# Kernel tuning notes

Measured on AMD Instinct MI355X. Metric: run time of the kernel, lower is better.

## Reference

```python
import jax, jax.numpy as jnp
import numpy as np

EPS = 1e-6

def _det3(m):
    return (m[..., 0, 0] * m[..., 1, 1] * m[..., 2, 2]
            + m[..., 0, 1] * m[..., 1, 2] * m[..., 2, 0]
            + m[..., 1, 0] * m[..., 2, 1] * m[..., 0, 2]
            - m[..., 2, 0] * m[..., 1, 1] * m[..., 0, 2]
            - m[..., 0, 0] * m[..., 2, 1] * m[..., 1, 2]
            - m[..., 1, 0] * m[..., 0, 1] * m[..., 2, 2])

def _inv3(m):
    a, b, c = m[..., 0, 0], m[..., 0, 1], m[..., 0, 2]
    d, e, f = m[..., 1, 0], m[..., 1, 1], m[..., 1, 2]
    g, h, i = m[..., 2, 0], m[..., 2, 1], m[..., 2, 2]
    adj = jnp.stack([
        jnp.stack([e * i - f * h, c * h - b * i, b * f - c * e], -1),
        jnp.stack([f * g - d * i, a * i - c * g, c * d - a * f], -1),
        jnp.stack([d * h - e * g, b * g - a * h, a * e - b * d], -1)], -2)
    return adj / _det3(m)[..., None, None]

def setup_inputs() -> dict:
    key = jax.random.key(0)
    ks = jax.random.split(key, 12)
    N, B, DH = 100000, 2048, 256
    idx = jnp.sort(jnp.concatenate([jnp.arange(B, dtype=jnp.int32),
                                    jax.random.randint(ks[0], (N - B,), 0, B, dtype=jnp.int32)]))
    return {
        "t": jax.random.uniform(ks[1], (B, 1), jnp.float32, 0.01, 0.99),
        "h": jax.random.normal(ks[2], (N, DH), jnp.float32),
        "pos": jax.random.normal(ks[3], (N, 3), jnp.float32),
        "eps_h": jax.random.normal(ks[4], (N, DH), jnp.float32),
        "eps_pos": jax.random.normal(ks[5], (N, 3), jnp.float32),
        "gparam_h": jax.random.normal(ks[6], (1, 1), jnp.float32),
        "gparam_pos": jax.random.normal(ks[7], (1, 1), jnp.float32),
        "W_mu": jax.random.normal(ks[8], (DH, DH), jnp.float32) / np.sqrt(DH),
        "W_r1": jax.random.normal(ks[9], (DH, 2 * DH), jnp.float32) / np.sqrt(DH),
        "W_r2": jax.random.normal(ks[10], (2 * DH, DH), jnp.float32) / np.sqrt(2 * DH),
        "index": idx,
        "num_graphs": B,
    }


def _forward(t, h, pos, eps_h, eps_pos, gparam_h, gparam_pos, W_mu, W_r1, W_r2, index, B):
    eye = jnp.eye(3, dtype=h.dtype)
    seg_sum = lambda x: jax.ops.segment_sum(x, index, num_segments=B)
    counts = seg_sum(jnp.ones((index.shape[0],), h.dtype))  # [B]

    def scatter_center(x):  # x - per-graph mean, gathered back
        mean = seg_sum(x) / counts[:, None]
        return x - mean[index]

    # volatility g(t): per-graph, gathered to nodes
    g_h = (0.1 + jax.nn.softplus(gparam_h) * t)[index]      # [N,1]
    g_pos = (0.1 + jax.nn.softplus(gparam_pos) * t)[index]  # [N,1]

    def f_net(t_, hh, pp):  # surrogate forward transformation f
        tn = t_[index]                                      # [N,1]
        mu_h = (hh @ W_mu) * (1.0 - tn)
        sigma_h = 0.1 + 0.9 * tn                            # [N,1]
        mu_pos = pp * (1.0 - tn)
        nrm = pp / (jnp.linalg.norm(pp, axis=-1, keepdims=True) + EPS)
        a = (0.2 + 0.8 * tn)[..., None]                     # [N,1,1]
        b = (0.1 * tn)[..., None]
        U = a * eye + b * (nrm[:, :, None] * nrm[:, None, :])  # [N,3,3]
        return mu_h, sigma_h, mu_pos, U

    def z_pos_fn(mu, U, eps):
        return mu + scatter_center(jnp.einsum('nij,nj->ni', U, eps))

    def score_pos_fn(eps, U, inv_U=None, C=None):
        if inv_U is None or C is None:
            inv_U = _inv3(U)
            inv_V = _inv3(seg_sum(inv_U))
            C = inv_V[index] @ (inv_U - eye)
        y = jnp.einsum('nji,nj->ni', inv_U, eps)
        ybar = seg_sum(y)
        c = jnp.einsum('nji,nj->ni', C, ybar[index])
        return scatter_center(c - y)  # zero_cog_score=True

    def solve_pos_fn(U, prel):
        inv_U = _inv3(U)
        inv_V = _inv3(seg_sum(inv_U))
        C = inv_V[index] @ (inv_U - eye)
        c = seg_sum(jnp.einsum('nij,nj->ni', C, prel))[index]
        eps = jnp.einsum('nij,nj->ni', inv_U, prel - c)
        return eps, inv_U, C

    bdrift = lambda dz, score, g: dz - 0.5 * g ** 2 * score

    # ---- target backward drift (time_derivative via jvp over t) ----
    (mu_h, sig_h, mu_p, U), (dmu_h, dsig_h, dmu_p, dU) = jax.jvp(
        lambda tt: f_net(tt, h, pos), (t,), (jnp.ones_like(t),))
    z_h = mu_h + sig_h * eps_h
    dz_h = dmu_h + dsig_h * eps_h
    z_p = z_pos_fn(mu_p, U, eps_pos)
    dz_p = z_pos_fn(dmu_p, dU, eps_pos)
    tgt_h = bdrift(dz_h, -eps_h / sig_h, g_h)
    tgt_p = bdrift(dz_p, score_pos_fn(eps_pos, U), g_pos)

    # ---- approximate backward drift ('x0' parameterization) ----
    h_r = jnp.tanh(z_h @ W_r1) @ W_r2   # reconstructor r
    pos_r = z_p * 0.9
    (mu_h2, sig_h2, mu_p2, U2), (dmu_h2, dsig_h2, dmu_p2, dU2) = jax.jvp(
        lambda tt: f_net(tt, h_r, pos_r), (t,), (jnp.ones_like(t),))
    eps_h2 = (z_h - mu_h2) / sig_h2
    eps_p2, inv_U2, C2 = solve_pos_fn(U2, z_p - mu_p2)
    dz_h2 = dmu_h2 + dsig_h2 * eps_h2
    dz_p2 = z_pos_fn(dmu_p2, dU2, eps_p2)
    apx_h = bdrift(dz_h2, -eps_h2 / sig_h2, g_h)
    apx_p = bdrift(dz_p2, score_pos_fn(eps_p2, U2, inv_U2, C2), g_pos)

    # ---- 'simple' loss: mse(approx/g, target/g) ----
    loss_h = jnp.mean(((apx_h - tgt_h) / g_h) ** 2)
    loss_p = jnp.mean(((apx_p - tgt_p) / g_pos) ** 2)
    return loss_h, loss_p


def reference(t, h, pos, eps_h, eps_pos, gparam_h, gparam_pos, W_mu, W_r1, W_r2, index, num_graphs):
    return _forward(t, h, pos, eps_h, eps_pos, gparam_h, gparam_pos, W_mu, W_r1, W_r2, index, num_graphs)
```

## Files before the change

### kernel.cpp

```cpp
#include <hip/hip_runtime.h>
#include <math.h>

#define NTHREADS 256
#define EPSC 1e-6f
#define NPL 3

typedef short bf16x8 __attribute__((ext_vector_type(8)));
typedef float f32x4  __attribute__((ext_vector_type(4)));

__device__ __forceinline__ ushort f2bf(float x) {
  union { float f; unsigned u; } v; v.f = x;
  unsigned r = v.u + 0x7FFFu + ((v.u >> 16) & 1u);
  return (ushort)(r >> 16);
}
__device__ __forceinline__ float bf2f(ushort x) {
  union { unsigned u; float f; } v; v.u = ((unsigned)x) << 16;
  return v.f;
}
__device__ __forceinline__ float tanh_fast(float x) {
  float xc = fminf(fmaxf(x, -15.f), 15.f);
  float e = __expf(2.f * xc);
  return (e - 1.f) / (e + 1.f);
}

__device__ __forceinline__ void inv3x3(const float m[9], float o[9]) {
  float a=m[0],b=m[1],c=m[2],d=m[3],e=m[4],f=m[5],g=m[6],h=m[7],i=m[8];
  float det = a*e*i + b*f*g + d*h*c - g*e*c - a*h*f - d*b*i;
  float r = 1.0f/det;
  o[0]=(e*i-f*h)*r; o[1]=(c*h-b*i)*r; o[2]=(b*f-c*e)*r;
  o[3]=(f*g-d*i)*r; o[4]=(a*i-c*g)*r; o[5]=(c*d-a*f)*r;
  o[6]=(d*h-e*g)*r; o[7]=(b*g-a*h)*r; o[8]=(a*e-b*d)*r;
}

__device__ __forceinline__ float wred(float v) {
#pragma unroll
  for (int o = 32; o > 0; o >>= 1) v += __shfl_xor(v, o, 64);
  return v;
}

__device__ __forceinline__ void block_reduce_atomic(double v, double* target) {
#pragma unroll
  for (int off = 32; off > 0; off >>= 1) v += __shfl_down(v, off, 64);
  __shared__ double sm[NTHREADS/64];
  int lane = threadIdx.x & 63, wv = threadIdx.x >> 6;
  if (lane == 0) sm[wv] = v;
  __syncthreads();
  if (threadIdx.x == 0) {
    double s = 0.0;
#pragma unroll
    for (int i = 0; i < NTHREADS/64; ++i) s += sm[i];
    atomicAdd(target, s);
  }
}

__global__ __launch_bounds__(64) void pos_fused(
    int N, const float* __restrict__ pos, const float* __restrict__ epsp,
    const int* __restrict__ index, const float* __restrict__ t,
    const float* __restrict__ gpp, double* __restrict__ lossp)
{
  const int b = blockIdx.x;
  const int lane = threadIdx.x;

  int lo = 0, hi = N;
  while (lo < hi) { int mid = (lo + hi) >> 1; if (index[mid] < b) lo = mid + 1; else hi = mid; }
  const int start = lo;
  hi = N;
  while (lo < hi) { int mid = (lo + hi) >> 1; if (index[mid] < b + 1) lo = mid + 1; else hi = mid; }
  const int end = lo;
  const int cnt = end - start;
  const float fn = (float)cnt, rc = 1.0f / fn;

  const float tn  = t[b];
  const float a1  = 0.2f + 0.8f*tn, b1 = 0.1f*tn;
  const float omt = 1.0f - tn;
  const float sp  = log1pf(expf(gpp[0]));
  const float gp  = 0.1f + sp*tn;
  const float hg  = 0.5f*gp*gp;
  const float rgp = 1.0f/gp;
  const float pscale = 1.0f - 0.9f*omt;

  float iU[NPL][9], yv[NPL][3], wv[NPL][3], dwv[NPL][3], pv[NPL][3];
  float Vs[9] = {0}, wb[3] = {0}, dwb[3] = {0}, yb[3] = {0};
#pragma unroll
  for (int k = 0; k < NPL; ++k) {
    const int n = start + k*64 + lane;
    if (n < end) {
      const float px = pos[3*(size_t)n+0], py = pos[3*(size_t)n+1], pz = pos[3*(size_t)n+2];
      const float ex = epsp[3*(size_t)n+0], ey = epsp[3*(size_t)n+1], ez = epsp[3*(size_t)n+2];
      pv[k][0]=px; pv[k][1]=py; pv[k][2]=pz;
      const float pn = sqrtf(px*px+py*py+pz*pz) + EPSC;
      const float nx = px/pn, ny = py/pn, nz = pz/pn;
      const float nd = nx*ex + ny*ey + nz*ez;
      wv[k][0]=a1*ex + b1*nd*nx; wv[k][1]=a1*ey + b1*nd*ny; wv[k][2]=a1*ez + b1*nd*nz;
      dwv[k][0]=0.8f*ex + 0.1f*nd*nx; dwv[k][1]=0.8f*ey + 0.1f*nd*ny; dwv[k][2]=0.8f*ez + 0.1f*nd*nz;
      const float U[9] = { a1 + b1*nx*nx, b1*nx*ny,      b1*nx*nz,
                           b1*ny*nx,      a1 + b1*ny*ny, b1*ny*nz,
                           b1*nz*nx,      b1*nz*ny,      a1 + b1*nz*nz };
      inv3x3(U, iU[k]);
      yv[k][0] = iU[k][0]*ex + iU[k][3]*ey + iU[k][6]*ez;
      yv[k][1] = iU[k][1]*ex + iU[k][4]*ey + iU[k][7]*ez;
      yv[k][2] = iU[k][2]*ex + iU[k][5]*ey + iU[k][8]*ez;
#pragma unroll
      for (int j = 0; j < 9; ++j) Vs[j] += iU[k][j];
#pragma unroll
      for (int j = 0; j < 3; ++j) { wb[j]+=wv[k][j]; dwb[j]+=dwv[k][j]; yb[j]+=yv[k][j]; }
    }
  }
#pragma unroll
  for (int j = 0; j < 9; ++j) Vs[j] = wred(Vs[j]);
#pragma unroll
  for (int j = 0; j < 3; ++j) { wb[j]=wred(wb[j]); dwb[j]=wred(dwb[j]); yb[j]=wred(yb[j]); }

  float iV[9]; inv3x3(Vs, iV);
  float wm[3], dwm[3], u1[3], s1m[3];
#pragma unroll
  for (int i = 0; i < 3; ++i) { wm[i] = wb[i]*rc; dwm[i] = dwb[i]*rc; }
#pragma unroll
  for (int i = 0; i < 3; ++i) u1[i] = iV[0*3+i]*yb[0] + iV[1*3+i]*yb[1] + iV[2*3+i]*yb[2];
#pragma unroll
  for (int i = 0; i < 3; ++i) {
    const float csy = Vs[0*3+i]*u1[0] + Vs[1*3+i]*u1[1] + Vs[2*3+i]*u1[2] - fn*u1[i];
    s1m[i] = (csy - yb[i]) * rc;
  }

  float tg[NPL][3], zp[NPL][3], iU2[NPL][9], qv[NPL][3];
  float Vs2[9] = {0}, qs[3] = {0}, ps[3] = {0};
#pragma unroll
  for (int k = 0; k < NPL; ++k) {
    const int n = start + k*64 + lane;
    if (n < end) {
#pragma unroll
      for (int i = 0; i < 3; ++i) {
        const float c1 = iU[k][0*3+i]*u1[0] + iU[k][1*3+i]*u1[1] + iU[k][2*3+i]*u1[2] - u1[i];
        const float score1 = c1 - yv[k][i] - s1m[i];
        tg[k][i] = -pv[k][i] + dwv[k][i] - dwm[i] - hg*score1;
        zp[k][i] = pv[k][i]*omt + wv[k][i] - wm[i];
      }
      const float rx = 0.9f*zp[k][0], ry = 0.9f*zp[k][1], rz = 0.9f*zp[k][2];
      const float rn = sqrtf(rx*rx+ry*ry+rz*rz) + EPSC;
      const float nx = rx/rn, ny = ry/rn, nz = rz/rn;
      const float U2[9] = { a1 + b1*nx*nx, b1*nx*ny,      b1*nx*nz,
                            b1*ny*nx,      a1 + b1*ny*ny, b1*ny*nz,
                            b1*nz*nx,      b1*nz*ny,      a1 + b1*nz*nz };
      inv3x3(U2, iU2[k]);
      float prel[3];
#pragma unroll
      for (int i = 0; i < 3; ++i) prel[i] = zp[k][i]*pscale;
#pragma unroll
      for (int i = 0; i < 3; ++i)
        qv[k][i] = iU2[k][i*3+0]*prel[0] + iU2[k][i*3+1]*prel[1] + iU2[k][i*3+2]*prel[2];
#pragma unroll
      for (int j = 0; j < 9; ++j) Vs2[j] += iU2[k][j];
#pragma unroll
      for (int j = 0; j < 3; ++j) { qs[j] += qv[k][j]; ps[j] += prel[j]; }
    }
  }
#pragma unroll
  for (int j = 0; j < 9; ++j) Vs2[j] = wred(Vs2[j]);
#pragma unroll
  for (int j = 0; j < 3; ++j) { qs[j] = wred(qs[j]); ps[j] = wred(ps[j]); }

  float iV2[9]; inv3x3(Vs2, iV2);
  float cb2[3];
#pragma unroll
  for (int i = 0; i < 3; ++i)
    cb2[i] = iV2[i*3+0]*(qs[0]-ps[0]) + iV2[i*3+1]*(qs[1]-ps[1]) + iV2[i*3+2]*(qs[2]-ps[2]);

  float y2v[NPL][3], dw2v[NPL][3];
  float yb2[3] = {0}, dwb2[3] = {0};
#pragma unroll
  for (int k = 0; k < NPL; ++k) {
    const int n = start + k*64 + lane;
    if (n < end) {
      float e[3];
#pragma unroll
      for (int i = 0; i < 3; ++i)
        e[i] = qv[k][i] - (iU2[k][i*3+0]*cb2[0] + iU2[k][i*3+1]*cb2[1] + iU2[k][i*3+2]*cb2[2]);
#pragma unroll
      for (int i = 0; i < 3; ++i)
        y2v[k][i] = iU2[k][0*3+i]*e[0] + iU2[k][1*3+i]*e[1] + iU2[k][2*3+i]*e[2];
      const float rx = 0.9f*zp[k][0], ry = 0.9f*zp[k][1], rz = 0.9f*zp[k][2];
      const float rn = sqrtf(rx*rx+ry*ry+rz*rz) + EPSC;
      const float nx = rx/rn, ny = ry/rn, nz = rz/rn;
      const float nd = nx*e[0] + ny*e[1] + nz*e[2];
      dw2v[k][0] = 0.8f*e[0] + 0.1f*nd*nx;
      dw2v[k][1] = 0.8f*e[1] + 0.1f*nd*ny;
      dw2v[k][2] = 0.8f*e[2] + 0.1f*nd*nz;
#pragma unroll
      for (int j = 0; j < 3; ++j) { yb2[j] += y2v[k][j]; dwb2[j] += dw2v[k][j]; }
    }
  }
#pragma unroll
  for (int j = 0; j < 3; ++j) { yb2[j] = wred(yb2[j]); dwb2[j] = wred(dwb2[j]); }

  float u2[3], s2m[3], dw2m[3];
#pragma unroll
  for (int i = 0; i < 3; ++i) u2[i] = iV2[0*3+i]*yb2[0] + iV2[1*3+i]*yb2[1] + iV2[2*3+i]*yb2[2];
#pragma unroll
  for (int i = 0; i < 3; ++i) {
    const float csy = Vs2[0*3+i]*u2[0] + Vs2[1*3+i]*u2[1] + Vs2[2*3+i]*u2[2] - fn*u2[i];
    s2m[i] = (csy - yb2[i]) * rc;
    dw2m[i] = dwb2[i] * rc;
  }

  float acc = 0.0f;
#pragma unroll
  for (int k = 0; k < NPL; ++k) {
    const int n = start + k*64 + lane;
    if (n < end) {
#pragma unroll
      for (int i = 0; i < 3; ++i) {
        const float c2 = iU2[k][0*3+i]*u2[0] + iU2[k][1*3+i]*u2[1] + iU2[k][2*3+i]*u2[2] - u2[i];
        const float score2 = c2 - y2v[k][i] - s2m[i];
        const float dz2 = -0.9f*zp[k][i] + dw2v[k][i] - dw2m[i];
        const float apx = dz2 - hg*score2;
        const float d = (apx - tg[k][i]) * rgp;
        acc += d*d;
      }
    }
  }
  acc = wred(acc);
  if (lane == 0) atomicAdd(lossp, (double)acc);
}

__global__ __launch_bounds__(NTHREADS) void cvt_bf16(
    const float4* __restrict__ in, ushort4* __restrict__ out, int n4)
{
  for (int i = blockIdx.x*blockDim.x + threadIdx.x; i < n4; i += gridDim.x*blockDim.x) {
    float4 v = in[i];
    out[i] = make_ushort4(f2bf(v.x), f2bf(v.y), f2bf(v.z), f2bf(v.w));
  }
}

__global__ __launch_bounds__(NTHREADS) void transpose_cvt(
    const float* __restrict__ in, ushort* __restrict__ out, int K, int Nn)
{
  __shared__ float ts[32][33];
  const int tx = threadIdx.x & 31, ty = threadIdx.x >> 5;
  const int nb = blockIdx.x*32, kb = blockIdx.y*32;
#pragma unroll
  for (int r = 0; r < 4; ++r)
    ts[ty + r*8][tx] = in[(size_t)(kb + ty + r*8)*Nn + nb + tx];
  __syncthreads();
#pragma unroll
  for (int r = 0; r < 4; ++r)
    out[(size_t)(nb + ty + r*8)*K + kb + tx] = f2bf(ts[tx][ty + r*8]);
}

__global__ __launch_bounds__(256) void gemm_wcomb(
    const ushort* __restrict__ A, const ushort* __restrict__ Bt,
    int K, int Nn, int Mvalid, ushort* __restrict__ OutB)
{
  __shared__ __align__(16) ushort As[128*32];
  __shared__ __align__(16) ushort Bs[128*32];
  const int tid = threadIdx.x;
  const int row0 = blockIdx.y*128, col0 = blockIdx.x*128;
  const int wave = tid >> 6, lane = tid & 63;
  const int wm = (wave & 1)*64, wn = (wave >> 1)*64;
  const int lm = lane & 15, lq = lane >> 4;

  f32x4 acc[4][4];
#pragma unroll
  for (int i = 0; i < 4; ++i)
#pragma unroll
    for (int j = 0; j < 4; ++j) { acc[i][j][0]=0.f; acc[i][j][1]=0.f; acc[i][j][2]=0.f; acc[i][j][3]=0.f; }

  const int c0 = tid, c1 = tid + 256;
  const int r0a = c0 >> 2, k0a = (c0 & 3) << 3;
  const int r1a = c1 >> 2, k1a = (c1 & 3) << 3;

  for (int k0 = 0; k0 < K; k0 += 32) {
    __syncthreads();
    __builtin_amdgcn_global_load_lds(
        (const __attribute__((address_space(1))) void*)(A + (size_t)(row0 + r0a)*K + k0 + k0a),
        (__attribute__((address_space(3))) void*)(As + c0*8), 16, 0, 0);
    __builtin_amdgcn_global_load_lds(
        (const __attribute__((address_space(1))) void*)(A + (size_t)(row0 + r1a)*K + k0 + k1a),
        (__attribute__((address_space(3))) void*)(As + c1*8), 16, 0, 0);
    __builtin_amdgcn_global_load_lds(
        (const __attribute__((address_space(1))) void*)(Bt + (size_t)(col0 + r0a)*K + k0 + k0a),
        (__attribute__((address_space(3))) void*)(Bs + c0*8), 16, 0, 0);
    __builtin_amdgcn_global_load_lds(
        (const __attribute__((address_space(1))) void*)(Bt + (size_t)(col0 + r1a)*K + k0 + k1a),
        (__attribute__((address_space(3))) void*)(Bs + c1*8), 16, 0, 0);
    __syncthreads();

    bf16x8 af[4], bfr[4];
#pragma unroll
    for (int i = 0; i < 4; ++i)
      af[i] = *(const bf16x8*)&As[(wm + i*16 + lm)*32 + lq*8];
#pragma unroll
    for (int j = 0; j < 4; ++j)
      bfr[j] = *(const bf16x8*)&Bs[(wn + j*16 + lm)*32 + lq*8];
#pragma unroll
    for (int i = 0; i < 4; ++i)
#pragma unroll
      for (int j = 0; j < 4; ++j)
        acc[i][j] = __builtin_amdgcn_mfma_f32_16x16x32_bf16(af[i], bfr[j], acc[i][j], 0, 0, 0);
  }

#pragma unroll
  for (int i = 0; i < 4; ++i) {
#pragma unroll
    for (int reg = 0; reg < 4; ++reg) {
      const int r = row0 + wm + i*16 + lq*4 + reg;
#pragma unroll
      for (int j = 0; j < 4; ++j) {
        const int cc = col0 + wn + j*16 + lm;
        OutB[(size_t)cc*Mvalid + r] = f2bf(acc[i][j][reg]);
      }
    }
  }
}

__global__ __launch_bounds__(256, 2) void fused_h(
    const ushort* __restrict__ hb, const ushort* __restrict__ wmut,
    const ushort* __restrict__ wr1t, const ushort* __restrict__ wct,
    const float* __restrict__ eps, const int* __restrict__ index,
    const float* __restrict__ t, const float* __restrict__ gph,
    int N, double* __restrict__ lossAcc)
{
  __shared__ __align__(16) ushort zs[64*264];
  __shared__ __align__(16) ushort t1s[64*136];
  __shared__ __align__(16) ushort As1[64*32];
  __shared__ __align__(16) ushort Bs[256*32];

  const int tid = threadIdx.x;
  const int row0 = blockIdx.x * 64;
  const int wave = tid >> 6, lane = tid & 63;
  const int lm = lane & 15, lq = lane >> 4;
  const int wn  = wave * 64;
  const int wn2 = wave * 32;

  f32x4 acc1[4][4];
#pragma unroll
  for (int i = 0; i < 4; ++i)
#pragma unroll
    for (int j = 0; j < 4; ++j) { acc1[i][j][0]=0.f; acc1[i][j][1]=0.f; acc1[i][j][2]=0.f; acc1[i][j][3]=0.f; }

  const int ra = tid >> 2, ka = (tid & 3) << 3;

  for (int k0 = 0; k0 < 256; k0 += 32) {
    __syncthreads();
    __builtin_amdgcn_global_load_lds(
        (const __attribute__((address_space(1))) void*)(hb + (size_t)(row0 + ra)*256 + k0 + ka),
        (__attribute__((address_space(3))) void*)(As1 + tid*8), 16, 0, 0);
#pragma unroll
    for (int j = 0; j < 4; ++j) {
      const int c = tid + j*256;
      const int rb = c >> 2, kc = (c & 3) << 3;
      __builtin_amdgcn_global_load_lds(
          (const __attribute__((address_space(1))) void*)(wmut + (size_t)rb*256 + k0 + kc),
          (__attribute__((address_space(3))) void*)(Bs + c*8), 16, 0, 0);
    }
    __syncthreads();
    bf16x8 af[4], bfr[4];
#pragma unroll
    for (int i = 0; i < 4; ++i)
      af[i] = *(const bf16x8*)&As1[(i*16 + lm)*32 + lq*8];
#pragma unroll
    for (int j = 0; j < 4; ++j)
      bfr[j] = *(const bf16x8*)&Bs[(wn + j*16 + lm)*32 + lq*8];
#pragma unroll
    for (int i = 0; i < 4; ++i)
#pragma unroll
      for (int j = 0; j < 4; ++j)
        acc1[i][j] = __builtin_amdgcn_mfma_f32_16x16x32_bf16(af[i], bfr[j], acc1[i][j], 0, 0, 0);
  }

  unsigned hmp[4][4][2];
#pragma unroll
  for (int i = 0; i < 4; ++i) {
#pragma unroll
    for (int reg = 0; reg < 4; ++reg) {
      const int rb = i*16 + lq*4 + reg;
      const int r = row0 + rb;
      const int rcl = (r < N) ? r : (N - 1);
      const float tn = t[index[rcl]];
      const float s0 = 1.0f - tn, s1 = 0.1f + 0.9f*tn;
#pragma unroll
      for (int j = 0; j < 4; ++j) {
        const int cc = wn + j*16 + lm;
        const float hm = acc1[i][j][reg];
        const unsigned hb16 = (unsigned)f2bf(hm);
        if (reg & 1) hmp[i][j][reg >> 1] |= hb16 << 16;
        else         hmp[i][j][reg >> 1]  = hb16;
        const float z = hm*s0 + s1*eps[(size_t)rcl*256 + cc];
        zs[rb*264 + cc] = f2bf(z);
      }
    }
  }

  f32x4 accL[4][4];
#pragma unroll
  for (int i = 0; i < 4; ++i)
#pragma unroll
    for (int j = 0; j < 4; ++j) { accL[i][j][0]=0.f; accL[i][j][1]=0.f; accL[i][j][2]=0.f; accL[i][j][3]=0.f; }

  for (int c2 = 0; c2 < 4; ++c2) {
    f32x4 acct[4][2];
#pragma unroll
    for (int i = 0; i < 4; ++i)
#pragma unroll
      for (int j = 0; j < 2; ++j) { acct[i][j][0]=0.f; acct[i][j][1]=0.f; acct[i][j][2]=0.f; acct[i][j][3]=0.f; }

    for (int k0 = 0; k0 < 256; k0 += 32) {
      __syncthreads();
#pragma unroll
      for (int j = 0; j < 2; ++j) {
        const int c = tid + j*256;
        const int rb = c >> 2, kc = (c & 3) << 3;
        __builtin_amdgcn_global_load_lds(
            (const __attribute__((address_space(1))) void*)(wr1t + (size_t)(c2*128 + rb)*256 + k0 + kc),
            (__attribute__((address_space(3))) void*)(Bs + c*8), 16, 0, 0);
      }
      __syncthreads();
      bf16x8 af[4], bt[2];
#pragma unroll
      for (int i = 0; i < 4; ++i)
        af[i] = *(const bf16x8*)&zs[(i*16 + lm)*264 + k0 + lq*8];
#pragma unroll
      for (int j = 0; j < 2; ++j)
        bt[j] = *(const bf16x8*)&Bs[(wn2 + j*16 + lm)*32 + lq*8];
#pragma unroll
      for (int i = 0; i < 4; ++i)
#pragma unroll
        for (int j = 0; j < 2; ++j)
          acct[i][j] = __builtin_amdgcn_mfma_f32_16x16x32_bf16(af[i], bt[j], acct[i][j], 0, 0, 0);
    }
    __syncthreads();

#pragma unroll
    for (int i = 0; i < 4; ++i)
#pragma unroll
      for (int j = 0; j < 2; ++j)
#pragma unroll
        for (int reg = 0; reg < 4; ++reg) {
          const int rb = i*16 + lq*4 + reg;
          const int c = wn2 + j*16 + lm;
          t1s[rb*136 + c] = f2bf(tanh_fast(acct[i][j][reg]));
        }

    for (int k0 = 0; k0 < 128; k0 += 32) {
      __syncthreads();
#pragma unroll
      for (int j = 0; j < 4; ++j) {
        const int c = tid + j*256;
        const int rb = c >> 2, kc = (c & 3) << 3;
        __builtin_amdgcn_global_load_lds(
            (const __attribute__((address_space(1))) void*)(wct + (size_t)rb*512 + c2*128 + k0 + kc),
            (__attribute__((address_space(3))) void*)(Bs + c*8), 16, 0, 0);
      }
      __syncthreads();
      bf16x8 af[4], bfr[4];
#pragma unroll
      for (int i = 0; i < 4; ++i)
        af[i] = *(const bf16x8*)&t1s[(i*16 + lm)*136 + k0 + lq*8];
#pragma unroll
      for (int j = 0; j < 4; ++j)
        bfr[j] = *(const bf16x8*)&Bs[(wn + j*16 + lm)*32 + lq*8];
#pragma unroll
      for (int i = 0; i < 4; ++i)
#pragma unroll
        for (int j = 0; j < 4; ++j)
          accL[i][j] = __builtin_amdgcn_mfma_f32_16x16x32_bf16(af[i], bfr[j], accL[i][j], 0, 0, 0);
    }
  }

  const float sp = log1pf(expf(gph[0]));
  float local = 0.f;
#pragma unroll
  for (int i = 0; i < 4; ++i) {
#pragma unroll
    for (int reg = 0; reg < 4; ++reg) {
      const int rb = i*16 + lq*4 + reg;
      const int r = row0 + rb;
      if (r < N) {
        const float tn = t[index[r]];
        const float gh  = 0.1f + sp*tn;
        const float sig = 0.1f + 0.9f*tn;
        const float fac = 1.0f + (0.9f + 0.5f*gh*gh/sig)*(1.0f - tn)/sig;
        const float sc  = fac/gh;
#pragma unroll
        for (int j = 0; j < 4; ++j) {
          const unsigned pw = hmp[i][j][reg >> 1];
          const ushort hb16 = (reg & 1) ? (ushort)(pw >> 16) : (ushort)(pw & 0xffffu);
          const float d = (bf2f(hb16) - accL[i][j][reg]) * sc;
          local += d*d;
        }
      }
    }
  }
  block_reduce_atomic((double)local, lossAcc);
}

__global__ void finalize_kernel(const double* lossh, const double* lossp,
                                float* out, int N, int DH)
{
  if (threadIdx.x == 0) {
    out[0] = (float)(lossh[0] / ((double)N * (double)DH));
    out[1] = (float)(lossp[0] / ((double)N * 3.0));
  }
}

extern "C" void kernel_launch(void* const* d_in, const int* in_sizes, int n_in,
                              void* d_out, int out_size, void* d_ws, size_t ws_size,
                              hipStream_t stream) {
  const float* t      = (const float*)d_in[0];
  const float* h      = (const float*)d_in[1];
  const float* pos    = (const float*)d_in[2];
  const float* eps_h  = (const float*)d_in[3];
  const float* eps_p  = (const float*)d_in[4];
  const float* gph    = (const float*)d_in[5];
  const float* gpp    = (const float*)d_in[6];
  const float* W_mu   = (const float*)d_in[7];
  const float* W_r1   = (const float*)d_in[8];
  const float* W_r2   = (const float*)d_in[9];
  const int*   index  = (const int*)d_in[10];
  const int B = in_sizes[0];
  const int N = in_sizes[10];
  const int DH = 256, DH2 = 512;
  const int NPAD = 100352;

  char* ws = (char*)d_ws;
  size_t off = 0;
  auto alloc = [&](size_t nbytes) { size_t o = off; off += (nbytes + 255) & ~(size_t)255; return o; };

  size_t o_loss = alloc(16);
  size_t o_hb   = alloc((size_t)NPAD*DH*2);
  size_t o_wmut = alloc((size_t)DH*DH*2);
  size_t o_wr1t = alloc((size_t)DH2*DH*2);
  size_t o_wr2b = alloc((size_t)DH2*DH*2);
  size_t o_wct  = alloc((size_t)DH*DH2*2);

  hipMemsetAsync(ws + o_loss, 0, 16, stream);

  double* lossh = (double*)(ws + o_loss);
  double* lossp = lossh + 1;
  ushort* hb   = (ushort*)(ws + o_hb);
  ushort* wmut = (ushort*)(ws + o_wmut);
  ushort* wr1t = (ushort*)(ws + o_wr1t);
  ushort* wr2b = (ushort*)(ws + o_wr2b);
  ushort* wct  = (ushort*)(ws + o_wct);

  pos_fused<<<B, 64, 0, stream>>>(N, pos, eps_p, index, t, gpp, lossp);

  cvt_bf16<<<2048, NTHREADS, 0, stream>>>((const float4*)h, (ushort4*)hb, N*DH/4);
  cvt_bf16<<<128, NTHREADS, 0, stream>>>((const float4*)W_r2, (ushort4*)wr2b, DH2*DH/4);
  transpose_cvt<<<dim3(DH/32,  DH/32), NTHREADS, 0, stream>>>(W_mu, wmut, DH, DH);
  transpose_cvt<<<dim3(DH2/32, DH/32), NTHREADS, 0, stream>>>(W_r1, wr1t, DH, DH2);

  gemm_wcomb<<<dim3(DH/128, DH2/128), 256, 0, stream>>>(
      wr2b, wmut, DH, DH, DH2, wct);

  const int mg64 = (N + 63) / 64;
  fused_h<<<mg64, 256, 0, stream>>>(
      hb, wmut, wr1t, wct, eps_h, index, t, gph, N, lossh);

  finalize_kernel<<<1, 64, 0, stream>>>(lossh, lossp, (float*)d_out, N, DH);
}
```

Before: 457.2 us.

## Pipeline fused_h weight loads per wave with double-buffered LDS and swizzled tiles

Restructures the fused_h kernel so each wave stages its own slice of the weight tiles in a private double-buffered LDS region. It prefetches the next k-slice with global_load_lds and uses explicit vmcnt waits in place of block-wide barriers inside every k loop. The A operand of the first GEMM is loaded directly into registers, the z and tanh intermediates use XOR-swizzled LDS layouts in place of padding, and the final reduction becomes per-wave atomics. The aim is to overlap global loads with MFMA and remove barrier stalls, at the cost of more registers (af[8][4]) and fragile hand-tuned waitcnt counts.

```diff
diff --git a/kernel.cpp b/kernel.cpp
--- a/kernel.cpp
+++ b/kernel.cpp
@@ -7,6 +7,10 @@
 
 typedef short bf16x8 __attribute__((ext_vector_type(8)));
 typedef float f32x4  __attribute__((ext_vector_type(4)));
+
+#define GLDS(srcp, dstp) __builtin_amdgcn_global_load_lds( \
+    (const __attribute__((address_space(1))) void*)(srcp), \
+    (__attribute__((address_space(3))) void*)(dstp), 16, 0, 0)
 
 __device__ __forceinline__ ushort f2bf(float x) {
   union { float f; unsigned u; } v; v.f = x;
@@ -36,21 +40,6 @@
 #pragma unroll
   for (int o = 32; o > 0; o >>= 1) v += __shfl_xor(v, o, 64);
   return v;
-}
-
-__device__ __forceinline__ void block_reduce_atomic(double v, double* target) {
-#pragma unroll
-  for (int off = 32; off > 0; off >>= 1) v += __shfl_down(v, off, 64);
-  __shared__ double sm[NTHREADS/64];
-  int lane = threadIdx.x & 63, wv = threadIdx.x >> 6;
-  if (lane == 0) sm[wv] = v;
-  __syncthreads();
-  if (threadIdx.x == 0) {
-    double s = 0.0;
-#pragma unroll
-    for (int i = 0; i < NTHREADS/64; ++i) s += sm[i];
-    atomicAdd(target, s);
-  }
 }
 
 __global__ __launch_bounds__(64) void pos_fused(
@@ -271,18 +260,10 @@
 
   for (int k0 = 0; k0 < K; k0 += 32) {
     __syncthreads();
-    __builtin_amdgcn_global_load_lds(
-        (const __attribute__((address_space(1))) void*)(A + (size_t)(row0 + r0a)*K + k0 + k0a),
-        (__attribute__((address_space(3))) void*)(As + c0*8), 16, 0, 0);
-    __builtin_amdgcn_global_load_lds(
-        (const __attribute__((address_space(1))) void*)(A + (size_t)(row0 + r1a)*K + k0 + k1a),
-        (__attribute__((address_space(3))) void*)(As + c1*8), 16, 0, 0);
-    __builtin_amdgcn_global_load_lds(
-        (const __attribute__((address_space(1))) void*)(Bt + (size_t)(col0 + r0a)*K + k0 + k0a),
-        (__attribute__((address_space(3))) void*)(Bs + c0*8), 16, 0, 0);
-    __builtin_amdgcn_global_load_lds(
-        (const __attribute__((address_space(1))) void*)(Bt + (size_t)(col0 + r1a)*K + k0 + k1a),
-        (__attribute__((address_space(3))) void*)(Bs + c1*8), 16, 0, 0);
+    GLDS(A  + (size_t)(row0 + r0a)*K + k0 + k0a, As + c0*8);
+    GLDS(A  + (size_t)(row0 + r1a)*K + k0 + k1a, As + c1*8);
+    GLDS(Bt + (size_t)(col0 + r0a)*K + k0 + k0a, Bs + c0*8);
+    GLDS(Bt + (size_t)(col0 + r1a)*K + k0 + k1a, Bs + c1*8);
     __syncthreads();
 
     bf16x8 af[4], bfr[4];
@@ -320,10 +301,9 @@
     const float* __restrict__ t, const float* __restrict__ gph,
     int N, double* __restrict__ lossAcc)
 {
-  __shared__ __align__(16) ushort zs[64*264];
-  __shared__ __align__(16) ushort t1s[64*136];
-  __shared__ __align__(16) ushort As1[64*32];
-  __shared__ __align__(16) ushort Bs[256*32];
+  __shared__ __align__(16) ushort zs[64*256];
+  __shared__ __align__(16) ushort t1s[64*128];
+  __shared__ __align__(16) ushort bstg[4*4096];
 
   const int tid = threadIdx.x;
   const int row0 = blockIdx.x * 64;
@@ -331,6 +311,20 @@
   const int lm = lane & 15, lq = lane >> 4;
   const int wn  = wave * 64;
   const int wn2 = wave * 32;
+  ushort* const bsw = bstg + wave*4096;
+
+  bf16x8 af[8][4];
+#pragma unroll
+  for (int k = 0; k < 4; ++k)
+#pragma unroll
+    for (int i = 0; i < 4; ++i)
+      af[k][i] = *(const bf16x8*)(hb + (size_t)(row0 + i*16 + lm)*256 + k*32 + lq*8);
+
+#pragma unroll
+  for (int c = 0; c < 4; ++c) {
+    const int ch = c*64 + lane;
+    GLDS(wmut + (size_t)(wn + (ch>>2))*256 + ((ch&3)<<3), bsw + ch*8);
+  }
 
   f32x4 acc1[4][4];
 #pragma unroll
@@ -338,34 +332,42 @@
 #pragma unroll
     for (int j = 0; j < 4; ++j) { acc1[i][j][0]=0.f; acc1[i][j][1]=0.f; acc1[i][j][2]=0.f; acc1[i][j][3]=0.f; }
 
-  const int ra = tid >> 2, ka = (tid & 3) << 3;
-
-  for (int k0 = 0; k0 < 256; k0 += 32) {
-    __syncthreads();
-    __builtin_amdgcn_global_load_lds(
-        (const __attribute__((address_space(1))) void*)(hb + (size_t)(row0 + ra)*256 + k0 + ka),
-        (__attribute__((address_space(3))) void*)(As1 + tid*8), 16, 0, 0);
-#pragma unroll
-    for (int j = 0; j < 4; ++j) {
-      const int c = tid + j*256;
-      const int rb = c >> 2, kc = (c & 3) << 3;
-      __builtin_amdgcn_global_load_lds(
-          (const __attribute__((address_space(1))) void*)(wmut + (size_t)rb*256 + k0 + kc),
-          (__attribute__((address_space(3))) void*)(Bs + c*8), 16, 0, 0);
-    }
-    __syncthreads();
-    bf16x8 af[4], bfr[4];
+#pragma unroll
+  for (int k = 0; k < 8; ++k) {
+    if (k < 4) {
+#pragma unroll
+      for (int i = 0; i < 4; ++i)
+        af[k+4][i] = *(const bf16x8*)(hb + (size_t)(row0 + i*16 + lm)*256 + (k+4)*32 + lq*8);
+    }
+    if (k < 7) {
+#pragma unroll
+      for (int c = 0; c < 4; ++c) {
+        const int ch = c*64 + lane;
+        GLDS(wmut + (size_t)(wn + (ch>>2))*256 + (k+1)*32 + ((ch&3)<<3),
+             bsw + ((k+1)&1)*2048 + ch*8);
+      }
+    }
+    if (k < 4)      { asm volatile("s_waitcnt vmcnt(8)" ::: "memory"); }
+    else if (k < 7) { asm volatile("s_waitcnt vmcnt(4)" ::: "memory"); }
+    else            { asm volatile("s_waitcnt vmcnt(0)" ::: "memory"); }
+    __builtin_amdgcn_sched_barrier(0);
+
+    const ushort* cb = bsw + (k&1)*2048;
+    bf16x8 bfr[4];
+#pragma unroll
+    for (int j = 0; j < 4; ++j)
+      bfr[j] = *(const bf16x8*)&cb[(j*16 + lm)*32 + lq*8];
 #pragma unroll
     for (int i = 0; i < 4; ++i)
-      af[i] = *(const bf16x8*)&As1[(i*16 + lm)*32 + lq*8];
-#pragma unroll
-    for (int j = 0; j < 4; ++j)
-      bfr[j] = *(const bf16x8*)&Bs[(wn + j*16 + lm)*32 + lq*8];
-#pragma unroll
-    for (int i = 0; i < 4; ++i)
 #pragma unroll
       for (int j = 0; j < 4; ++j)
-        acc1[i][j] = __builtin_amdgcn_mfma_f32_16x16x32_bf16(af[i], bfr[j], acc1[i][j], 0, 0, 0);
+        acc1[i][j] = __builtin_amdgcn_mfma_f32_16x16x32_bf16(af[k][i], bfr[j], acc1[i][j], 0, 0, 0);
+  }
+
+#pragma unroll
+  for (int c = 0; c < 2; ++c) {
+    const int ch = c*64 + lane;
+    GLDS(wr1t + (size_t)(wn2 + (ch>>2))*256 + ((ch&3)<<3), bsw + ch*8);
   }
 
   unsigned hmp[4][4][2];
@@ -382,14 +384,15 @@
       for (int j = 0; j < 4; ++j) {
         const int cc = wn + j*16 + lm;
         const float hm = acc1[i][j][reg];
-        const unsigned hb16 = (unsigned)f2bf(hm);
-        if (reg & 1) hmp[i][j][reg >> 1] |= hb16 << 16;
-        else         hmp[i][j][reg >> 1]  = hb16;
+        const unsigned hv = (unsigned)f2bf(hm);
+        if (reg & 1) hmp[i][j][reg >> 1] |= hv << 16;
+        else         hmp[i][j][reg >> 1]  = hv;
         const float z = hm*s0 + s1*eps[(size_t)rcl*256 + cc];
-        zs[rb*264 + cc] = f2bf(z);
-      }
-    }
-  }
+        zs[rb*256 + (cc ^ ((rb & 7) << 3))] = f2bf(z);
+      }
+    }
+  }
+  __syncthreads();
 
   f32x4 accL[4][4];
 #pragma unroll
@@ -404,29 +407,43 @@
 #pragma unroll
       for (int j = 0; j < 2; ++j) { acct[i][j][0]=0.f; acct[i][j][1]=0.f; acct[i][j][2]=0.f; acct[i][j][3]=0.f; }
 
-    for (int k0 = 0; k0 < 256; k0 += 32) {
-      __syncthreads();
-#pragma unroll
-      for (int j = 0; j < 2; ++j) {
-        const int c = tid + j*256;
-        const int rb = c >> 2, kc = (c & 3) << 3;
-        __builtin_amdgcn_global_load_lds(
-            (const __attribute__((address_space(1))) void*)(wr1t + (size_t)(c2*128 + rb)*256 + k0 + kc),
-            (__attribute__((address_space(3))) void*)(Bs + c*8), 16, 0, 0);
-      }
-      __syncthreads();
-      bf16x8 af[4], bt[2];
+#pragma unroll
+    for (int k = 0; k < 8; ++k) {
+      if (k < 7) {
+#pragma unroll
+        for (int c = 0; c < 2; ++c) {
+          const int ch = c*64 + lane;
+          GLDS(wr1t + (size_t)(c2*128 + wn2 + (ch>>2))*256 + (k+1)*32 + ((ch&3)<<3),
+               bsw + ((k+1)&1)*2048 + ch*8);
+        }
+        asm volatile("s_waitcnt vmcnt(2)" ::: "memory");
+      } else {
+        asm volatile("s_waitcnt vmcnt(0)" ::: "memory");
+      }
+      __builtin_amdgcn_sched_barrier(0);
+
+      const ushort* cb = bsw + (k&1)*2048;
+      bf16x8 azf[4], bfr[2];
+#pragma unroll
+      for (int i = 0; i < 4; ++i) {
+        const int r = i*16 + lm;
+        const int c = k*32 + lq*8;
+        azf[i] = *(const bf16x8*)&zs[r*256 + (c ^ ((r & 7) << 3))];
+      }
+#pragma unroll
+      for (int j = 0; j < 2; ++j)
+        bfr[j] = *(const bf16x8*)&cb[(j*16 + lm)*32 + lq*8];
 #pragma unroll
       for (int i = 0; i < 4; ++i)
-        af[i] = *(const bf16x8*)&zs[(i*16 + lm)*264 + k0 + lq*8];
-#pragma unroll
-      for (int j = 0; j < 2; ++j)
-        bt[j] = *(const bf16x8*)&Bs[(wn2 + j*16 + lm)*32 + lq*8];
-#pragma unroll
-      for (int i = 0; i < 4; ++i)
 #pragma unroll
         for (int j = 0; j < 2; ++j)
-          acct[i][j] = __builtin_amdgcn_mfma_f32_16x16x32_bf16(af[i], bt[j], acct[i][j], 0, 0, 0);
+          acct[i][j] = __builtin_amdgcn_mfma_f32_16x16x32_bf16(azf[i], bfr[j], acct[i][j], 0, 0, 0);
+    }
+
+#pragma unroll
+    for (int c = 0; c < 4; ++c) {
+      const int ch = c*64 + lane;
+      GLDS(wct + (size_t)(wn + (ch>>2))*512 + c2*128 + ((ch&3)<<3), bsw + ch*8);
     }
     __syncthreads();
 
@@ -438,32 +455,49 @@
         for (int reg = 0; reg < 4; ++reg) {
           const int rb = i*16 + lq*4 + reg;
           const int c = wn2 + j*16 + lm;
-          t1s[rb*136 + c] = f2bf(tanh_fast(acct[i][j][reg]));
+          t1s[rb*128 + (c ^ ((rb & 7) << 3))] = f2bf(tanh_fast(acct[i][j][reg]));
         }
-
-    for (int k0 = 0; k0 < 128; k0 += 32) {
-      __syncthreads();
-#pragma unroll
-      for (int j = 0; j < 4; ++j) {
-        const int c = tid + j*256;
-        const int rb = c >> 2, kc = (c & 3) << 3;
-        __builtin_amdgcn_global_load_lds(
-            (const __attribute__((address_space(1))) void*)(wct + (size_t)rb*512 + c2*128 + k0 + kc),
-            (__attribute__((address_space(3))) void*)(Bs + c*8), 16, 0, 0);
-      }
-      __syncthreads();
-      bf16x8 af[4], bfr[4];
+    __syncthreads();
+
+#pragma unroll
+    for (int k = 0; k < 4; ++k) {
+      if (k < 3) {
+#pragma unroll
+        for (int c = 0; c < 4; ++c) {
+          const int ch = c*64 + lane;
+          GLDS(wct + (size_t)(wn + (ch>>2))*512 + c2*128 + (k+1)*32 + ((ch&3)<<3),
+               bsw + ((k+1)&1)*2048 + ch*8);
+        }
+        asm volatile("s_waitcnt vmcnt(4)" ::: "memory");
+      } else {
+        asm volatile("s_waitcnt vmcnt(0)" ::: "memory");
+      }
+      __builtin_amdgcn_sched_barrier(0);
+
+      const ushort* cb = bsw + (k&1)*2048;
+      bf16x8 atf[4], bfr[4];
+#pragma unroll
+      for (int i = 0; i < 4; ++i) {
+        const int r = i*16 + lm;
+        const int c = k*32 + lq*8;
+        atf[i] = *(const bf16x8*)&t1s[r*128 + (c ^ ((r & 7) << 3))];
+      }
+#pragma unroll
+      for (int j = 0; j < 4; ++j)
+        bfr[j] = *(const bf16x8*)&cb[(j*16 + lm)*32 + lq*8];
 #pragma unroll
       for (int i = 0; i < 4; ++i)
-        af[i] = *(const bf16x8*)&t1s[(i*16 + lm)*136 + k0 + lq*8];
-#pragma unroll
-      for (int j = 0; j < 4; ++j)
-        bfr[j] = *(const bf16x8*)&Bs[(wn + j*16 + lm)*32 + lq*8];
-#pragma unroll
-      for (int i = 0; i < 4; ++i)
 #pragma unroll
         for (int j = 0; j < 4; ++j)
-          accL[i][j] = __builtin_amdgcn_mfma_f32_16x16x32_bf16(af[i], bfr[j], accL[i][j], 0, 0, 0);
+          accL[i][j] = __builtin_amdgcn_mfma_f32_16x16x32_bf16(atf[i], bfr[j], accL[i][j], 0, 0, 0);
+    }
+
+    if (c2 < 3) {
+#pragma unroll
+      for (int c = 0; c < 2; ++c) {
+        const int ch = c*64 + lane;
+        GLDS(wr1t + (size_t)((c2+1)*128 + wn2 + (ch>>2))*256 + ((ch&3)<<3), bsw + ch*8);
+      }
     }
   }
 
@@ -484,14 +518,17 @@
 #pragma unroll
         for (int j = 0; j < 4; ++j) {
           const unsigned pw = hmp[i][j][reg >> 1];
-          const ushort hb16 = (reg & 1) ? (ushort)(pw >> 16) : (ushort)(pw & 0xffffu);
-          const float d = (bf2f(hb16) - accL[i][j][reg]) * sc;
+          const ushort hv = (reg & 1) ? (ushort)(pw >> 16) : (ushort)(pw & 0xffffu);
+          const float d = (bf2f(hv) - accL[i][j][reg]) * sc;
           local += d*d;
         }
       }
     }
   }
-  block_reduce_atomic((double)local, lossAcc);
+  double dv = (double)local;
+#pragma unroll
+  for (int off = 32; off > 0; off >>= 1) dv += __shfl_down(dv, off, 64);
+  if (lane == 0) atomicAdd(lossAcc, dv);
 }
 
 __global__ void finalize_kernel(const double* lossh, const double* lossp,
```

Result: slower. 478.9 us (+4.8%).
